# Kernel tuning notes

Measured on AMD Instinct MI355X. Metric: run time of the kernel, lower is better.

Reference implementation:

```python
import jax, jax.numpy as jnp
import numpy as np
import math

B, T, N_CTX, H = 4, 512, 2048, 1024
NUM_HEADS, NUM_INSTRUMENTS, MAX_BARS = 16, 16, 8
HEAD_DIM = H // NUM_HEADS


def setup_inputs() -> dict:
    key = jax.random.key(0)
    ks = jax.random.split(key, 16)
    s = 1.0 / math.sqrt(H)
    return {
        "query": jax.random.normal(ks[0], (B, T, H), jnp.float32),
        "context": jax.random.normal(ks[1], (B, N_CTX, H), jnp.float32),
        "instrument_ids": jax.random.randint(ks[2], (B, N_CTX), 0, NUM_INSTRUMENTS),
        "current_instrument_id": 3,
        "bar_offsets": jax.random.randint(ks[3], (B, N_CTX), 0, MAX_BARS),
        "Wq": jax.random.normal(ks[4], (H, H), jnp.float32) * s,
        "bq": jnp.zeros((H,), jnp.float32),
        "Wk": jax.random.normal(ks[5], (H, H), jnp.float32) * s,
        "bk": jnp.zeros((H,), jnp.float32),
        "Wv": jax.random.normal(ks[6], (H, H), jnp.float32) * s,
        "bv": jnp.zeros((H,), jnp.float32),
        "Wo": jax.random.normal(ks[7], (H, H), jnp.float32) * s,
        "bo": jnp.zeros((H,), jnp.float32),
        "inst_emb": jax.random.normal(ks[8], (NUM_INSTRUMENTS, H), jnp.float32),
        "bar_emb": jax.random.normal(ks[9], (MAX_BARS, H), jnp.float32),
    }


def reference(query, context, instrument_ids, current_instrument_id, bar_offsets,
              Wq, bq, Wk, bk, Wv, bv, Wo, bo, inst_emb, bar_emb):
    # current_instrument_id: python int -> broadcast to (B,)
    cur = jnp.full((B,), current_instrument_id, dtype=jnp.int64 if instrument_ids.dtype == jnp.int64 else jnp.int32)
    # add embeddings to query and context
    q = query + inst_emb[cur][:, None, :]                              # (B,T,H)
    ctx = context + inst_emb[instrument_ids] + bar_emb[jnp.clip(bar_offsets, 0, MAX_BARS - 1)]  # (B,N,H)
    # projections (torch Linear: x @ W.T + b)
    Q = (q @ Wq.T + bq).reshape(B, T, NUM_HEADS, HEAD_DIM).transpose(0, 2, 1, 3)      # (B,h,T,d)
    K = (ctx @ Wk.T + bk).reshape(B, N_CTX, NUM_HEADS, HEAD_DIM).transpose(0, 2, 1, 3)  # (B,h,N,d)
    V = (ctx @ Wv.T + bv).reshape(B, N_CTX, NUM_HEADS, HEAD_DIM).transpose(0, 2, 1, 3)  # (B,h,N,d)
    scores = jnp.einsum('bhtd,bhnd->bhtn', Q, K) / math.sqrt(HEAD_DIM)  # (B,h,T,N)
    # attend only to keys whose instrument differs from the current one
    keep = (instrument_ids != cur[:, None])[:, None, None, :]           # (B,1,1,N)
    scores = jnp.where(keep, scores, jnp.float32(-1e9))
    probs = jax.nn.softmax(scores, axis=-1)
    out = jnp.einsum('bhtn,bhnd->bhtd', probs, V).transpose(0, 2, 1, 3).reshape(B, T, H)
    return out @ Wo.T + bo
```

## Files before the change

kernel.cpp:

```cpp
#include <hip/hip_runtime.h>

#define H 1024
#define B_ 4
#define T_ 512
#define NCTX 2048
#define NH 16
#define HD 64

typedef __attribute__((ext_vector_type(8))) short bf16x8;
typedef __attribute__((ext_vector_type(4))) float f32x4;
typedef __attribute__((ext_vector_type(4))) short s16x4;

__device__ __forceinline__ ushort f2b(float f) {
  union { float f; unsigned u; } v; v.f = f;
  unsigned u = v.u;
  unsigned r = (u + 0x7FFFu + ((u >> 16) & 1u)) >> 16;
  return (ushort)r;
}

__device__ __forceinline__ void gld16(const void* g, void* l) {
  __builtin_amdgcn_global_load_lds((const __attribute__((address_space(1))) unsigned int*)g,
                                   (__attribute__((address_space(3))) unsigned int*)l, 16, 0, 0);
}


__global__ void cvt_kernel(const float* __restrict__ src, ushort* __restrict__ dst) {
  int i = blockIdx.x * blockDim.x + threadIdx.x;
  float4 v = ((const float4*)src)[i];
  s16x4 o;
  o[0] = (short)f2b(v.x); o[1] = (short)f2b(v.y);
  o[2] = (short)f2b(v.z); o[3] = (short)f2b(v.w);
  ((s16x4*)dst)[i] = o;
}

__global__ void prep_q_kernel(const float* __restrict__ q, const float* __restrict__ iemb,
                              const int* __restrict__ curp, ushort* __restrict__ out) {
  int cur = curp[0];
  int i = blockIdx.x * blockDim.x + threadIdx.x;
  int c4 = i & 255;
  float4 v = ((const float4*)q)[i];
  float4 e = ((const float4*)(iemb + (size_t)cur * H))[c4];
  s16x4 o;
  o[0] = (short)f2b(v.x + e.x); o[1] = (short)f2b(v.y + e.y);
  o[2] = (short)f2b(v.z + e.z); o[3] = (short)f2b(v.w + e.w);
  ((s16x4*)out)[i] = o;
}

__global__ void prep_ctx_kernel(const float* __restrict__ ctx, const float* __restrict__ iemb,
                                const float* __restrict__ bemb, const int* __restrict__ ids,
                                const int* __restrict__ bars, ushort* __restrict__ out) {
  int i = blockIdx.x * blockDim.x + threadIdx.x;
  int row = i >> 8;
  int c4 = i & 255;
  int id = ids[row];
  int bar = bars[row];
  bar = bar < 0 ? 0 : (bar > 7 ? 7 : bar);
  float4 v = ((const float4*)ctx)[i];
  float4 e = ((const float4*)(iemb + (size_t)id * H))[c4];
  float4 g = ((const float4*)(bemb + (size_t)bar * H))[c4];
  s16x4 o;
  o[0] = (short)f2b(v.x + e.x + g.x); o[1] = (short)f2b(v.y + e.y + g.y);
  o[2] = (short)f2b(v.z + e.z + g.z); o[3] = (short)f2b(v.w + e.w + g.w);
  ((s16x4*)out)[i] = o;
}


template <int MODE>
__global__ __launch_bounds__(256) void gemm_k(const ushort* __restrict__ A,
                                              const ushort* __restrict__ W,
                                              const float* __restrict__ bias,
                                              void* __restrict__ Cout) {
  __shared__ ushort As[128 * 32];
  __shared__ ushort Bs[128 * 32];
  const int tid = threadIdx.x;
  const int lane = tid & 63;
  const int wv = tid >> 6;
  const int wr = wv >> 1, wc = wv & 1;
  const int lo = lane & 15, hi = lane >> 4;
  const int row0 = blockIdx.y * 128, col0 = blockIdx.x * 128;

  f32x4 acc[4][4];
#pragma unroll
  for (int m = 0; m < 4; m++)
#pragma unroll
    for (int n = 0; n < 4; n++) acc[m][n] = (f32x4){0.f, 0.f, 0.f, 0.f};

  for (int kt = 0; kt < H; kt += 32) {
#pragma unroll
    for (int c = 0; c < 2; c++) {
      int ia = wv * 128 + c * 64 + lane;
      int r = ia >> 2, s = ia & 3;
      gld16(A + (size_t)(row0 + r) * H + kt + s * 8, (char*)As + (wv * 128 + c * 64) * 16);
      gld16(W + (size_t)(col0 + r) * H + kt + s * 8, (char*)Bs + (wv * 128 + c * 64) * 16);
    }
    __syncthreads();
    bf16x8 af[4], bfr[4];
#pragma unroll
    for (int m = 0; m < 4; m++) af[m] = *(const bf16x8*)(As + (wr * 64 + m * 16 + lo) * 32 + hi * 8);
#pragma unroll
    for (int n = 0; n < 4; n++) bfr[n] = *(const bf16x8*)(Bs + (wc * 64 + n * 16 + lo) * 32 + hi * 8);
#pragma unroll
    for (int m = 0; m < 4; m++)
#pragma unroll
      for (int n = 0; n < 4; n++)
        acc[m][n] = __builtin_amdgcn_mfma_f32_16x16x32_bf16(af[m], bfr[n], acc[m][n], 0, 0, 0);
    __syncthreads();
  }

#pragma unroll
  for (int m = 0; m < 4; m++) {
    int gr0 = row0 + wr * 64 + m * 16 + hi * 4;
#pragma unroll
    for (int n = 0; n < 4; n++) {
      int gc = col0 + wc * 64 + n * 16 + lo;
      float bv = bias[gc];
      if (MODE == 0) {
        ushort* C = (ushort*)Cout;
#pragma unroll
        for (int r = 0; r < 4; r++)
          C[(size_t)(gr0 + r) * H + gc] = f2b(acc[m][n][r] + bv);
      } else if (MODE == 1) {
        ushort* C = (ushort*)Cout;
        int bb = gr0 >> 11, n0 = gr0 & 2047;
        s16x4 o;
#pragma unroll
        for (int r = 0; r < 4; r++) o[r] = (short)f2b(acc[m][n][r] + bv);
        *(s16x4*)(C + (size_t)bb * (H * NCTX) + (size_t)gc * NCTX + n0) = o;
      } else {
        float* C = (float*)Cout;
#pragma unroll
        for (int r = 0; r < 4; r++)
          C[(size_t)(gr0 + r) * H + gc] = acc[m][n][r] + bv;
      }
    }
  }
}


__global__ __launch_bounds__(256) void attn_k(const ushort* __restrict__ Q,
                                              const ushort* __restrict__ K,
                                              const ushort* __restrict__ VT,
                                              const int* __restrict__ ids,
                                              const int* __restrict__ curp,
                                              ushort* __restrict__ O) {
  __shared__ ushort Ks[64 * 64];
  __shared__ ushort Vs[64 * 64];
  __shared__ ushort Ps[4][16 * 64];
  const int blk = (blockIdx.x & 7) * 64 + (blockIdx.x >> 3);
  const int qt = blk & 7;
  const int h = (blk >> 3) & 15;
  const int b = blk >> 7;
  const int cur = curp[0];
  const int tid = threadIdx.x, lane = tid & 63, w = tid >> 6;
  const int lo = lane & 15, hi = lane >> 4;
  const int swz = (lo & 7) << 4;

  const ushort* Qp = Q + ((size_t)(b * T_ + qt * 64 + w * 16 + lo)) * H + h * HD;
  bf16x8 qf0 = *(const bf16x8*)(Qp + hi * 8);
  bf16x8 qf1 = *(const bf16x8*)(Qp + 32 + hi * 8);

  f32x4 oacc[4];
#pragma unroll
  for (int d = 0; d < 4; d++) oacc[d] = (f32x4){0.f, 0.f, 0.f, 0.f};
  float mrow = -1e30f, lrow = 0.f;

  const int* idb = ids + b * NCTX;

  for (int kv0 = 0; kv0 < NCTX; kv0 += 64) {
#pragma unroll
    for (int i = 0; i < 2; i++) {
      int seg = tid + i * 256;
      int r = seg >> 3, s = seg & 7;
      int wb = (r * 128 + s * 16) ^ ((r & 7) << 4);
      *(bf16x8*)((char*)Ks + wb) =
          *(const bf16x8*)(K + ((size_t)(b * NCTX + kv0 + r)) * H + h * HD + s * 8);
      *(bf16x8*)((char*)Vs + wb) =
          *(const bf16x8*)(VT + (size_t)b * (H * NCTX) + (size_t)(h * HD + r) * NCTX + kv0 + s * 8);
    }
    __syncthreads();

    f32x4 sc[4];
#pragma unroll
    for (int nt = 0; nt < 4; nt++) {
      bf16x8 kf0 = *(const bf16x8*)((char*)Ks + ((((nt * 16 + lo) * 128) + hi * 16) ^ swz));
      bf16x8 kf1 = *(const bf16x8*)((char*)Ks + ((((nt * 16 + lo) * 128) + 64 + hi * 16) ^ swz));
      f32x4 z = (f32x4){0.f, 0.f, 0.f, 0.f};
      z = __builtin_amdgcn_mfma_f32_16x16x32_bf16(kf0, qf0, z, 0, 0, 0);
      sc[nt] = __builtin_amdgcn_mfma_f32_16x16x32_bf16(kf1, qf1, z, 0, 0, 0);
    }

    float p[4][4];
#pragma unroll
    for (int nt = 0; nt < 4; nt++) {
      int4 iv = *(const int4*)(idb + kv0 + nt * 16 + hi * 4);
      p[nt][0] = (iv.x != cur) ? sc[nt][0] * 0.125f : -1e30f;
      p[nt][1] = (iv.y != cur) ? sc[nt][1] * 0.125f : -1e30f;
      p[nt][2] = (iv.z != cur) ? sc[nt][2] * 0.125f : -1e30f;
      p[nt][3] = (iv.w != cur) ? sc[nt][3] * 0.125f : -1e30f;
    }

    float x = fmaxf(fmaxf(fmaxf(p[0][0], p[0][1]), fmaxf(p[0][2], p[0][3])),
                    fmaxf(fmaxf(p[1][0], p[1][1]), fmaxf(p[1][2], p[1][3])));
    x = fmaxf(x, fmaxf(fmaxf(fmaxf(p[2][0], p[2][1]), fmaxf(p[2][2], p[2][3])),
                       fmaxf(fmaxf(p[3][0], p[3][1]), fmaxf(p[3][2], p[3][3]))));
    x = fmaxf(x, __shfl_xor(x, 16));
    x = fmaxf(x, __shfl_xor(x, 32));
    float mn = fmaxf(mrow, x);
    float scal = __expf(mrow - mn);
    mrow = mn;
    float rs = 0.f;
#pragma unroll
    for (int nt = 0; nt < 4; nt++)
#pragma unroll
      for (int r = 0; r < 4; r++) {
        float e = __expf(p[nt][r] - mn);
        p[nt][r] = e;
        rs += e;
      }
    rs += __shfl_xor(rs, 16);
    rs += __shfl_xor(rs, 32);
    lrow = lrow * scal + rs;

    float sq0 = __shfl(scal, hi * 4 + 0);
    float sq1 = __shfl(scal, hi * 4 + 1);
    float sq2 = __shfl(scal, hi * 4 + 2);
    float sq3 = __shfl(scal, hi * 4 + 3);
#pragma unroll
    for (int d = 0; d < 4; d++) {
      oacc[d][0] *= sq0; oacc[d][1] *= sq1; oacc[d][2] *= sq2; oacc[d][3] *= sq3;
    }

#pragma unroll
    for (int nt = 0; nt < 4; nt++) {
      s16x4 pw;
#pragma unroll
      for (int r = 0; r < 4; r++) pw[r] = (short)f2b(p[nt][r]);
      *(s16x4*)((char*)Ps[w] + ((lo * 128 + (nt * 16 + hi * 4) * 2) ^ swz)) = pw;
    }

#pragma unroll
    for (int ks = 0; ks < 2; ks++) {
      bf16x8 pa = *(const bf16x8*)((char*)Ps[w] + ((lo * 128 + (ks * 64 + hi * 16)) ^ swz));
#pragma unroll
      for (int d = 0; d < 4; d++) {
        bf16x8 vf = *(const bf16x8*)((char*)Vs + (((d * 16 + lo) * 128 + ks * 64 + hi * 16) ^ swz));
        oacc[d] = __builtin_amdgcn_mfma_f32_16x16x32_bf16(pa, vf, oacc[d], 0, 0, 0);
      }
    }
    __syncthreads();
  }

  float lr0 = __shfl(lrow, hi * 4 + 0);
  float lr1 = __shfl(lrow, hi * 4 + 1);
  float lr2 = __shfl(lrow, hi * 4 + 2);
  float lr3 = __shfl(lrow, hi * 4 + 3);
#pragma unroll
  for (int d = 0; d < 4; d++) {
    int t = qt * 64 + w * 16 + hi * 4;
    size_t base = ((size_t)(b * T_ + t)) * H + h * HD + d * 16 + lo;
    O[base] = f2b(oacc[d][0] / lr0);
    O[base + H] = f2b(oacc[d][1] / lr1);
    O[base + 2 * H] = f2b(oacc[d][2] / lr2);
    O[base + 3 * H] = f2b(oacc[d][3] / lr3);
  }
}


extern "C" void kernel_launch(void* const* d_in, const int* in_sizes, int n_in,
                              void* d_out, int out_size, void* d_ws, size_t ws_size,
                              hipStream_t stream) {
  const float* query = (const float*)d_in[0];
  const float* context = (const float*)d_in[1];
  const int* ids = (const int*)d_in[2];
  const int* curp = (const int*)d_in[3];
  const int* bars = (const int*)d_in[4];
  const float* Wq = (const float*)d_in[5];
  const float* bq = (const float*)d_in[6];
  const float* Wk = (const float*)d_in[7];
  const float* bk = (const float*)d_in[8];
  const float* Wv = (const float*)d_in[9];
  const float* bv = (const float*)d_in[10];
  const float* Wo = (const float*)d_in[11];
  const float* bo = (const float*)d_in[12];
  const float* iemb = (const float*)d_in[13];
  const float* bemb = (const float*)d_in[14];
  float* out = (float*)d_out;

  ushort* ws = (ushort*)d_ws;
  ushort* Wqb = ws;
  ushort* Wkb = Wqb + (1u << 20);
  ushort* Wvb = Wkb + (1u << 20);
  ushort* Wob = Wvb + (1u << 20);
  ushort* qin = Wob + (1u << 20);
  ushort* ctxb = qin + (2u << 20);
  ushort* Qb = ctxb + (8u << 20);
  ushort* Kb = Qb + (2u << 20);
  ushort* VTb = Kb + (8u << 20);
  ushort* AOb = VTb + (8u << 20);

  cvt_kernel<<<1024, 256, 0, stream>>>(Wq, Wqb);
  cvt_kernel<<<1024, 256, 0, stream>>>(Wk, Wkb);
  cvt_kernel<<<1024, 256, 0, stream>>>(Wv, Wvb);
  cvt_kernel<<<1024, 256, 0, stream>>>(Wo, Wob);
  prep_q_kernel<<<2048, 256, 0, stream>>>(query, iemb, curp, qin);
  prep_ctx_kernel<<<8192, 256, 0, stream>>>(context, iemb, bemb, ids, bars, ctxb);

  gemm_k<0><<<dim3(8, 16), 256, 0, stream>>>(qin, Wqb, bq, Qb);
  gemm_k<0><<<dim3(8, 64), 256, 0, stream>>>(ctxb, Wkb, bk, Kb);
  gemm_k<1><<<dim3(8, 64), 256, 0, stream>>>(ctxb, Wvb, bv, VTb);

  attn_k<<<512, 256, 0, stream>>>(Qb, Kb, VTb, ids, curp, AOb);

  gemm_k<2><<<dim3(8, 16), 256, 0, stream>>>(AOb, Wob, bo, out);
}
```

Before: 188.6 us.

## Split-KV attention with double buffering, fused KV GEMM, merged weight conversion

Merges the four weight conversion launches into one, folds the 1/sqrt(d) scale into the Q projection epilogue, and fuses the K and V projections into one GEMM that shares the A tile. Attention is split across two KV halves to double the block count, with register-staged double-buffered K/V loads and a lazy rescale that skips the correction when the row max grows by at most 8. A new combine kernel merges the two partials. The cost is extra fp32 partial traffic, one more launch, and higher register and LDS pressure in the fused GEMM.

Result: slower. 199.6 us (+5.8%).

```diff
diff --git a/kernel.cpp b/kernel.cpp
--- a/kernel.cpp
+++ b/kernel.cpp
@@ -24,13 +24,20 @@
 }
 
 
-__global__ void cvt_kernel(const float* __restrict__ src, ushort* __restrict__ dst) {
-  int i = blockIdx.x * blockDim.x + threadIdx.x;
-  float4 v = ((const float4*)src)[i];
+__global__ void cvt4_kernel(const float* __restrict__ s0, const float* __restrict__ s1,
+                            const float* __restrict__ s2, const float* __restrict__ s3,
+                            ushort* __restrict__ d0, ushort* __restrict__ d1,
+                            ushort* __restrict__ d2, ushort* __restrict__ d3) {
+  int blk = blockIdx.x;
+  int which = blk >> 10;
+  int i = (blk & 1023) * 256 + threadIdx.x;
+  const float* s = which == 0 ? s0 : which == 1 ? s1 : which == 2 ? s2 : s3;
+  ushort* d = which == 0 ? d0 : which == 1 ? d1 : which == 2 ? d2 : d3;
+  float4 v = ((const float4*)s)[i];
   s16x4 o;
   o[0] = (short)f2b(v.x); o[1] = (short)f2b(v.y);
   o[2] = (short)f2b(v.z); o[3] = (short)f2b(v.w);
-  ((s16x4*)dst)[i] = o;
+  ((s16x4*)d)[i] = o;
 }
 
 __global__ void prep_q_kernel(const float* __restrict__ q, const float* __restrict__ iemb,
@@ -65,7 +72,7 @@
 }
 
 
-template <int MODE>
+template <int MODE, int SCALE>
 __global__ __launch_bounds__(256) void gemm_k(const ushort* __restrict__ A,
                                               const ushort* __restrict__ W,
                                               const float* __restrict__ bias,
@@ -117,15 +124,11 @@
       if (MODE == 0) {
         ushort* C = (ushort*)Cout;
 #pragma unroll
-        for (int r = 0; r < 4; r++)
-          C[(size_t)(gr0 + r) * H + gc] = f2b(acc[m][n][r] + bv);
-      } else if (MODE == 1) {
-        ushort* C = (ushort*)Cout;
-        int bb = gr0 >> 11, n0 = gr0 & 2047;
-        s16x4 o;
-#pragma unroll
-        for (int r = 0; r < 4; r++) o[r] = (short)f2b(acc[m][n][r] + bv);
-        *(s16x4*)(C + (size_t)bb * (H * NCTX) + (size_t)gc * NCTX + n0) = o;
+        for (int r = 0; r < 4; r++) {
+          float x = acc[m][n][r] + bv;
+          if (SCALE) x *= 0.125f;
+          C[(size_t)(gr0 + r) * H + gc] = f2b(x);
+        }
       } else {
         float* C = (float*)Cout;
 #pragma unroll
@@ -136,24 +139,106 @@
   }
 }
 
+
+__global__ __launch_bounds__(256) void gemm_kv(const ushort* __restrict__ A,
+                                               const ushort* __restrict__ WK,
+                                               const ushort* __restrict__ WV,
+                                               const float* __restrict__ bK,
+                                               const float* __restrict__ bV,
+                                               ushort* __restrict__ Kout,
+                                               ushort* __restrict__ VTout) {
+  __shared__ ushort As[128 * 32];
+  __shared__ ushort BsK[128 * 32];
+  __shared__ ushort BsV[128 * 32];
+  const int tid = threadIdx.x;
+  const int lane = tid & 63;
+  const int wv = tid >> 6;
+  const int wr = wv >> 1, wc = wv & 1;
+  const int lo = lane & 15, hi = lane >> 4;
+  const int row0 = blockIdx.y * 128, col0 = blockIdx.x * 128;
+
+  f32x4 acck[4][4], accv[4][4];
+#pragma unroll
+  for (int m = 0; m < 4; m++)
+#pragma unroll
+    for (int n = 0; n < 4; n++) {
+      acck[m][n] = (f32x4){0.f, 0.f, 0.f, 0.f};
+      accv[m][n] = (f32x4){0.f, 0.f, 0.f, 0.f};
+    }
+
+  for (int kt = 0; kt < H; kt += 32) {
+#pragma unroll
+    for (int c = 0; c < 2; c++) {
+      int ia = wv * 128 + c * 64 + lane;
+      int r = ia >> 2, s = ia & 3;
+      int lb = (wv * 128 + c * 64) * 16;
+      gld16(A + (size_t)(row0 + r) * H + kt + s * 8, (char*)As + lb);
+      gld16(WK + (size_t)(col0 + r) * H + kt + s * 8, (char*)BsK + lb);
+      gld16(WV + (size_t)(col0 + r) * H + kt + s * 8, (char*)BsV + lb);
+    }
+    __syncthreads();
+    bf16x8 af[4], bk4[4], bv4[4];
+#pragma unroll
+    for (int m = 0; m < 4; m++) af[m] = *(const bf16x8*)(As + (wr * 64 + m * 16 + lo) * 32 + hi * 8);
+#pragma unroll
+    for (int n = 0; n < 4; n++) {
+      bk4[n] = *(const bf16x8*)(BsK + (wc * 64 + n * 16 + lo) * 32 + hi * 8);
+      bv4[n] = *(const bf16x8*)(BsV + (wc * 64 + n * 16 + lo) * 32 + hi * 8);
+    }
+#pragma unroll
+    for (int m = 0; m < 4; m++)
+#pragma unroll
+      for (int n = 0; n < 4; n++) {
+        acck[m][n] = __builtin_amdgcn_mfma_f32_16x16x32_bf16(af[m], bk4[n], acck[m][n], 0, 0, 0);
+        accv[m][n] = __builtin_amdgcn_mfma_f32_16x16x32_bf16(af[m], bv4[n], accv[m][n], 0, 0, 0);
+      }
+    __syncthreads();
+  }
+
+#pragma unroll
+  for (int m = 0; m < 4; m++) {
+    int gr0 = row0 + wr * 64 + m * 16 + hi * 4;
+    int bb = gr0 >> 11, n0 = gr0 & 2047;
+#pragma unroll
+    for (int n = 0; n < 4; n++) {
+      int gc = col0 + wc * 64 + n * 16 + lo;
+      float bvk = bK[gc], bvv = bV[gc];
+#pragma unroll
+      for (int r = 0; r < 4; r++)
+        Kout[(size_t)(gr0 + r) * H + gc] = f2b(acck[m][n][r] + bvk);
+      s16x4 o;
+#pragma unroll
+      for (int r = 0; r < 4; r++) o[r] = (short)f2b(accv[m][n][r] + bvv);
+      *(s16x4*)(VTout + (size_t)bb * (H * NCTX) + (size_t)gc * NCTX + n0) = o;
+    }
+  }
+}
+
+
+#define NSPLIT 2
+#define KVLEN (NCTX / NSPLIT)
+#define NT_KV (KVLEN / 64)
 
 __global__ __launch_bounds__(256) void attn_k(const ushort* __restrict__ Q,
                                               const ushort* __restrict__ K,
                                               const ushort* __restrict__ VT,
                                               const int* __restrict__ ids,
                                               const int* __restrict__ curp,
-                                              ushort* __restrict__ O) {
-  __shared__ ushort Ks[64 * 64];
-  __shared__ ushort Vs[64 * 64];
+                                              float* __restrict__ OPf,
+                                              float* __restrict__ mlf) {
+  __shared__ ushort Ks[2][64 * 64];
+  __shared__ ushort Vs[2][64 * 64];
   __shared__ ushort Ps[4][16 * 64];
-  const int blk = (blockIdx.x & 7) * 64 + (blockIdx.x >> 3);
+  const int blk = (blockIdx.x & 7) * 128 + (blockIdx.x >> 3);
   const int qt = blk & 7;
   const int h = (blk >> 3) & 15;
-  const int b = blk >> 7;
+  const int b = (blk >> 7) & 3;
+  const int p = blk >> 9;
   const int cur = curp[0];
   const int tid = threadIdx.x, lane = tid & 63, w = tid >> 6;
   const int lo = lane & 15, hi = lane >> 4;
   const int swz = (lo & 7) << 4;
+  const int kvbase = p * KVLEN;
 
   const ushort* Qp = Q + ((size_t)(b * T_ + qt * 64 + w * 16 + lo)) * H + h * HD;
   bf16x8 qf0 = *(const bf16x8*)(Qp + hi * 8);
@@ -165,76 +250,108 @@
   float mrow = -1e30f, lrow = 0.f;
 
   const int* idb = ids + b * NCTX;
-
-  for (int kv0 = 0; kv0 < NCTX; kv0 += 64) {
-#pragma unroll
-    for (int i = 0; i < 2; i++) {
-      int seg = tid + i * 256;
-      int r = seg >> 3, s = seg & 7;
-      int wb = (r * 128 + s * 16) ^ ((r & 7) << 4);
-      *(bf16x8*)((char*)Ks + wb) =
-          *(const bf16x8*)(K + ((size_t)(b * NCTX + kv0 + r)) * H + h * HD + s * 8);
-      *(bf16x8*)((char*)Vs + wb) =
-          *(const bf16x8*)(VT + (size_t)b * (H * NCTX) + (size_t)(h * HD + r) * NCTX + kv0 + s * 8);
-    }
-    __syncthreads();
+  const ushort* Kbase = K + ((size_t)(b * NCTX)) * H + h * HD;
+  const ushort* Vbase = VT + (size_t)b * (H * NCTX) + (size_t)(h * HD) * NCTX;
+
+  const int sr = tid >> 3 + 0;
+  (void)sr;
+
+  bf16x8 kr[2], vr[2];
+#pragma unroll
+  for (int i = 0; i < 2; i++) {
+    int seg = tid + i * 256;
+    int r = seg >> 3, s = seg & 7;
+    kr[i] = *(const bf16x8*)(Kbase + (size_t)(kvbase + r) * H + s * 8);
+    vr[i] = *(const bf16x8*)(Vbase + (size_t)r * NCTX + kvbase + s * 8);
+  }
+#pragma unroll
+  for (int i = 0; i < 2; i++) {
+    int seg = tid + i * 256;
+    int r = seg >> 3, s = seg & 7;
+    int wb = (r * 128 + s * 16) ^ ((r & 7) << 4);
+    *(bf16x8*)((char*)Ks[0] + wb) = kr[i];
+    *(bf16x8*)((char*)Vs[0] + wb) = vr[i];
+  }
+  __syncthreads();
+
+  int curbuf = 0;
+  for (int t = 0; t < NT_KV; t++) {
+    int kvt = kvbase + t * 64;
+    if (t < NT_KV - 1) {
+#pragma unroll
+      for (int i = 0; i < 2; i++) {
+        int seg = tid + i * 256;
+        int r = seg >> 3, s = seg & 7;
+        kr[i] = *(const bf16x8*)(Kbase + (size_t)(kvt + 64 + r) * H + s * 8);
+        vr[i] = *(const bf16x8*)(Vbase + (size_t)r * NCTX + kvt + 64 + s * 8);
+      }
+    }
 
     f32x4 sc[4];
 #pragma unroll
     for (int nt = 0; nt < 4; nt++) {
-      bf16x8 kf0 = *(const bf16x8*)((char*)Ks + ((((nt * 16 + lo) * 128) + hi * 16) ^ swz));
-      bf16x8 kf1 = *(const bf16x8*)((char*)Ks + ((((nt * 16 + lo) * 128) + 64 + hi * 16) ^ swz));
+      bf16x8 kf0 = *(const bf16x8*)((char*)Ks[curbuf] + ((((nt * 16 + lo) * 128) + hi * 16) ^ swz));
+      bf16x8 kf1 = *(const bf16x8*)((char*)Ks[curbuf] + ((((nt * 16 + lo) * 128) + 64 + hi * 16) ^ swz));
       f32x4 z = (f32x4){0.f, 0.f, 0.f, 0.f};
       z = __builtin_amdgcn_mfma_f32_16x16x32_bf16(kf0, qf0, z, 0, 0, 0);
       sc[nt] = __builtin_amdgcn_mfma_f32_16x16x32_bf16(kf1, qf1, z, 0, 0, 0);
     }
 
-    float p[4][4];
+    float pv[4][4];
 #pragma unroll
     for (int nt = 0; nt < 4; nt++) {
-      int4 iv = *(const int4*)(idb + kv0 + nt * 16 + hi * 4);
-      p[nt][0] = (iv.x != cur) ? sc[nt][0] * 0.125f : -1e30f;
-      p[nt][1] = (iv.y != cur) ? sc[nt][1] * 0.125f : -1e30f;
-      p[nt][2] = (iv.z != cur) ? sc[nt][2] * 0.125f : -1e30f;
-      p[nt][3] = (iv.w != cur) ? sc[nt][3] * 0.125f : -1e30f;
-    }
-
-    float x = fmaxf(fmaxf(fmaxf(p[0][0], p[0][1]), fmaxf(p[0][2], p[0][3])),
-                    fmaxf(fmaxf(p[1][0], p[1][1]), fmaxf(p[1][2], p[1][3])));
-    x = fmaxf(x, fmaxf(fmaxf(fmaxf(p[2][0], p[2][1]), fmaxf(p[2][2], p[2][3])),
-                       fmaxf(fmaxf(p[3][0], p[3][1]), fmaxf(p[3][2], p[3][3]))));
+      int4 iv = *(const int4*)(idb + kvt + nt * 16 + hi * 4);
+      pv[nt][0] = (iv.x != cur) ? sc[nt][0] : -1e30f;
+      pv[nt][1] = (iv.y != cur) ? sc[nt][1] : -1e30f;
+      pv[nt][2] = (iv.z != cur) ? sc[nt][2] : -1e30f;
+      pv[nt][3] = (iv.w != cur) ? sc[nt][3] : -1e30f;
+    }
+
+    float x = fmaxf(fmaxf(fmaxf(pv[0][0], pv[0][1]), fmaxf(pv[0][2], pv[0][3])),
+                    fmaxf(fmaxf(pv[1][0], pv[1][1]), fmaxf(pv[1][2], pv[1][3])));
+    x = fmaxf(x, fmaxf(fmaxf(fmaxf(pv[2][0], pv[2][1]), fmaxf(pv[2][2], pv[2][3])),
+                       fmaxf(fmaxf(pv[3][0], pv[3][1]), fmaxf(pv[3][2], pv[3][3]))));
     x = fmaxf(x, __shfl_xor(x, 16));
     x = fmaxf(x, __shfl_xor(x, 32));
-    float mn = fmaxf(mrow, x);
-    float scal = __expf(mrow - mn);
-    mrow = mn;
+    bool defer = __all((x <= mrow + 8.0f) && (mrow > -1e29f));
+    float mn, scal = 1.f;
+    if (defer) {
+      mn = mrow;
+    } else {
+      mn = fmaxf(mrow, x);
+      scal = __expf(mrow - mn);
+      mrow = mn;
+    }
     float rs = 0.f;
 #pragma unroll
     for (int nt = 0; nt < 4; nt++)
 #pragma unroll
       for (int r = 0; r < 4; r++) {
-        float e = __expf(p[nt][r] - mn);
-        p[nt][r] = e;
+        float e = __expf(pv[nt][r] - mn);
+        pv[nt][r] = e;
         rs += e;
       }
     rs += __shfl_xor(rs, 16);
     rs += __shfl_xor(rs, 32);
-    lrow = lrow * scal + rs;
-
-    float sq0 = __shfl(scal, hi * 4 + 0);
-    float sq1 = __shfl(scal, hi * 4 + 1);
-    float sq2 = __shfl(scal, hi * 4 + 2);
-    float sq3 = __shfl(scal, hi * 4 + 3);
-#pragma unroll
-    for (int d = 0; d < 4; d++) {
-      oacc[d][0] *= sq0; oacc[d][1] *= sq1; oacc[d][2] *= sq2; oacc[d][3] *= sq3;
+    if (defer) {
+      lrow += rs;
+    } else {
+      lrow = lrow * scal + rs;
+      float sq0 = __shfl(scal, hi * 4 + 0);
+      float sq1 = __shfl(scal, hi * 4 + 1);
+      float sq2 = __shfl(scal, hi * 4 + 2);
+      float sq3 = __shfl(scal, hi * 4 + 3);
+#pragma unroll
+      for (int d = 0; d < 4; d++) {
+        oacc[d][0] *= sq0; oacc[d][1] *= sq1; oacc[d][2] *= sq2; oacc[d][3] *= sq3;
+      }
     }
 
 #pragma unroll
     for (int nt = 0; nt < 4; nt++) {
       s16x4 pw;
 #pragma unroll
-      for (int r = 0; r < 4; r++) pw[r] = (short)f2b(p[nt][r]);
+      for (int r = 0; r < 4; r++) pw[r] = (short)f2b(pv[nt][r]);
       *(s16x4*)((char*)Ps[w] + ((lo * 128 + (nt * 16 + hi * 4) * 2) ^ swz)) = pw;
     }
 
@@ -243,26 +360,60 @@
       bf16x8 pa = *(const bf16x8*)((char*)Ps[w] + ((lo * 128 + (ks * 64 + hi * 16)) ^ swz));
 #pragma unroll
       for (int d = 0; d < 4; d++) {
-        bf16x8 vf = *(const bf16x8*)((char*)Vs + (((d * 16 + lo) * 128 + ks * 64 + hi * 16) ^ swz));
+        bf16x8 vf = *(const bf16x8*)((char*)Vs[curbuf] + (((d * 16 + lo) * 128 + ks * 64 + hi * 16) ^ swz));
         oacc[d] = __builtin_amdgcn_mfma_f32_16x16x32_bf16(pa, vf, oacc[d], 0, 0, 0);
       }
     }
+
+    if (t < NT_KV - 1) {
+#pragma unroll
+      for (int i = 0; i < 2; i++) {
+        int seg = tid + i * 256;
+        int r = seg >> 3, s = seg & 7;
+        int wb = (r * 128 + s * 16) ^ ((r & 7) << 4);
+        *(bf16x8*)((char*)Ks[curbuf ^ 1] + wb) = kr[i];
+        *(bf16x8*)((char*)Vs[curbuf ^ 1] + wb) = vr[i];
+      }
+    }
     __syncthreads();
-  }
-
-  float lr0 = __shfl(lrow, hi * 4 + 0);
-  float lr1 = __shfl(lrow, hi * 4 + 1);
-  float lr2 = __shfl(lrow, hi * 4 + 2);
-  float lr3 = __shfl(lrow, hi * 4 + 3);
+    curbuf ^= 1;
+  }
+
+  int row0 = b * 512 + qt * 64 + w * 16 + hi * 4;
 #pragma unroll
   for (int d = 0; d < 4; d++) {
-    int t = qt * 64 + w * 16 + hi * 4;
-    size_t base = ((size_t)(b * T_ + t)) * H + h * HD + d * 16 + lo;
-    O[base] = f2b(oacc[d][0] / lr0);
-    O[base + H] = f2b(oacc[d][1] / lr1);
-    O[base + 2 * H] = f2b(oacc[d][2] / lr2);
-    O[base + 3 * H] = f2b(oacc[d][3] / lr3);
-  }
+#pragma unroll
+    for (int r = 0; r < 4; r++)
+      OPf[((size_t)p * 2048 + row0 + r) * 1024 + h * 64 + d * 16 + lo] = oacc[d][r];
+  }
+  if (hi == 0) {
+    int qrow = b * 512 + qt * 64 + w * 16 + lo;
+    mlf[(((size_t)p * 2048 + qrow) * 16 + h) * 2] = mrow;
+    mlf[(((size_t)p * 2048 + qrow) * 16 + h) * 2 + 1] = lrow;
+  }
+}
+
+__global__ void attn_combine(const float* __restrict__ OPf, const float* __restrict__ mlf,
+                             ushort* __restrict__ O) {
+  int idx = blockIdx.x * 256 + threadIdx.x;
+  int btr = idx >> 8;
+  int c4 = idx & 255;
+  int h = c4 >> 4;
+  float m0 = mlf[((size_t)btr * 16 + h) * 2];
+  float l0 = mlf[((size_t)btr * 16 + h) * 2 + 1];
+  float m1 = mlf[(((size_t)2048 + btr) * 16 + h) * 2];
+  float l1 = mlf[(((size_t)2048 + btr) * 16 + h) * 2 + 1];
+  float M = fmaxf(m0, m1);
+  float a0 = __expf(m0 - M), a1 = __expf(m1 - M);
+  float inv = 1.0f / (a0 * l0 + a1 * l1);
+  float4 o0 = ((const float4*)OPf)[idx];
+  float4 o1 = ((const float4*)OPf)[(size_t)524288 + idx];
+  s16x4 r;
+  r[0] = (short)f2b((a0 * o0.x + a1 * o1.x) * inv);
+  r[1] = (short)f2b((a0 * o0.y + a1 * o1.y) * inv);
+  r[2] = (short)f2b((a0 * o0.z + a1 * o1.z) * inv);
+  r[3] = (short)f2b((a0 * o0.w + a1 * o1.w) * inv);
+  ((s16x4*)O)[idx] = r;
 }
 
 
@@ -298,18 +449,18 @@
   ushort* VTb = Kb + (8u << 20);
   ushort* AOb = VTb + (8u << 20);
 
-  cvt_kernel<<<1024, 256, 0, stream>>>(Wq, Wqb);
-  cvt_kernel<<<1024, 256, 0, stream>>>(Wk, Wkb);
-  cvt_kernel<<<1024, 256, 0, stream>>>(Wv, Wvb);
-  cvt_kernel<<<1024, 256, 0, stream>>>(Wo, Wob);
+  float* OPf = (float*)ctxb;
+  float* mlf = (float*)qin;
+
+  cvt4_kernel<<<4096, 256, 0, stream>>>(Wq, Wk, Wv, Wo, Wqb, Wkb, Wvb, Wob);
   prep_q_kernel<<<2048, 256, 0, stream>>>(query, iemb, curp, qin);
   prep_ctx_kernel<<<8192, 256, 0, stream>>>(context, iemb, bemb, ids, bars, ctxb);
 
-  gemm_k<0><<<dim3(8, 16), 256, 0, stream>>>(qin, Wqb, bq, Qb);
-  gemm_k<0><<<dim3(8, 64), 256, 0, stream>>>(ctxb, Wkb, bk, Kb);
-  gemm_k<1><<<dim3(8, 64), 256, 0, stream>>>(ctxb, Wvb, bv, VTb);
-
-  attn_k<<<512, 256, 0, stream>>>(Qb, Kb, VTb, ids, curp, AOb);
-
-  gemm_k<2><<<dim3(8, 16), 256, 0, stream>>>(AOb, Wob, bo, out);
-}
+  gemm_k<0, 1><<<dim3(8, 16), 256, 0, stream>>>(qin, Wqb, bq, Qb);
+  gemm_kv<<<dim3(8, 64), 256, 0, stream>>>(ctxb, Wkb, Wvb, bk, bv, Kb, VTb);
+
+  attn_k<<<1024, 256, 0, stream>>>(Qb, Kb, VTb, ids, curp, OPf, mlf);
+  attn_combine<<<2048, 256, 0, stream>>>(OPf, mlf, AOb);
+
+  gemm_k<2, 0><<<dim3(8, 16), 256, 0, stream>>>(AOb, Wob, bo, out);
+}
```
